# Kernel optimization log

Measured on AMD Instinct MI355X. Metric: run time of the kernel, lower is better.

The kernel has to match this reference:

```python
import jax, jax.numpy as jnp
import numpy as np

N_NODES = 100000
N_EDGES = 1600000
N_GRAPHS = 1000
NODES_PER_GRAPH = 100  # batch vector is arange(N)//100: exactly 100 nodes per graph
HID = 32
MAX_Z = 1000
K = 30
D_LAT = HID * 3 + 1  # 97, total_latent_dim


def setup_inputs() -> dict:
    key = jax.random.key(0)
    ks = jax.random.split(key, 24)
    s = 1.0 / np.sqrt(HID)
    inp = {
        "z": jax.random.randint(ks[0], (N_NODES,), 0, MAX_Z, dtype=jnp.int32),
        "edge_index": jax.random.randint(ks[1], (2, N_EDGES), 0, N_NODES, dtype=jnp.int32),
        "batch": (jnp.arange(N_NODES, dtype=jnp.int32) // NODES_PER_GRAPH),
        "edge_weight": jax.random.uniform(ks[2], (N_EDGES,), jnp.float32, 0.1, 1.0),
        "z_emb": jax.random.normal(ks[3], (MAX_Z, HID), jnp.float32) * 0.1,
        # GCNConv stack: [32->32, 32->32, 32->32, 32->1]
        "Wg1": jax.random.normal(ks[4], (HID, HID)) * s,
        "bg1": jnp.zeros((HID,), jnp.float32),
        "Wg2": jax.random.normal(ks[5], (HID, HID)) * s,
        "bg2": jnp.zeros((HID,), jnp.float32),
        "Wg3": jax.random.normal(ks[6], (HID, HID)) * s,
        "bg3": jnp.zeros((HID,), jnp.float32),
        "Wg4": jax.random.normal(ks[7], (HID, 1)) * s,
        "bg4": jnp.zeros((1,), jnp.float32),
        # Conv1d(1, 16, kernel=97, stride=97)
        "Wc1": jax.random.normal(ks[8], (16, D_LAT)) * (1.0 / np.sqrt(D_LAT)),
        "bc1": jnp.zeros((16,), jnp.float32),
        # Conv1d(16, 32, kernel=5, stride=1)
        "Wc2": jax.random.normal(ks[9], (32, 16, 5)) * (1.0 / np.sqrt(16 * 5)),
        "bc2": jnp.zeros((32,), jnp.float32),
        # Linear(352, 128), Linear(128, 1)
        "Wl1": jax.random.normal(ks[10], (352, 128)) * (1.0 / np.sqrt(352)),
        "bl1": jnp.zeros((128,), jnp.float32),
        "Wl2": jax.random.normal(ks[11], (128, 1)) * (1.0 / np.sqrt(128)),
        "bl2": jnp.zeros((1,), jnp.float32),
    }
    return inp


def gcn_conv(x, src, dst, ew, W, b, n):
    # PyG GCNConv: xW, add self-loops (weight 1), sym-normalize, aggregate at dst, + bias
    xw = x @ W
    deg = jax.ops.segment_sum(ew, dst, num_segments=n) + 1.0  # +1 for self loop
    dinv = jnp.where(deg > 0, jax.lax.rsqrt(deg), 0.0)
    norm = dinv[src] * ew * dinv[dst]                          # [E]
    out = jax.ops.segment_sum(norm[:, None] * xw[src], dst, num_segments=n)
    out = out + xw * (dinv * dinv)[:, None]                    # self-loop term
    return out + b


def _forward(z, edge_index, batch, edge_weight, z_emb, Wg1, bg1, Wg2, bg2, Wg3, bg3,
             Wg4, bg4, Wc1, bc1, Wc2, bc2, Wl1, bl1, Wl2, bl2):
    src, dst = edge_index[0], edge_index[1]
    n = z.shape[0]
    x = z_emb[z]                                              # [N, 32]
    xs = []
    h = x
    for W, b in ((Wg1, bg1), (Wg2, bg2), (Wg3, bg3), (Wg4, bg4)):
        h = jnp.tanh(gcn_conv(h, src, dst, edge_weight, W, b, n))
        xs.append(h)
    x = jnp.concatenate(xs, axis=-1)                          # [N, 97]
    # global_sort_pool: batch is uniform (100 nodes/graph) so dense batching is a reshape
    dense = x.reshape(N_GRAPHS, NODES_PER_GRAPH, D_LAT)       # [B, 100, 97]
    idx = jnp.argsort(-dense[:, :, -1], axis=1)[:, :K]        # sort desc by last channel
    top = jnp.take_along_axis(dense, idx[:, :, None], axis=1)  # [B, 30, 97]
    # Conv1d(1,16,97,stride=97) on flattened [B,1,30*97] == per-slot dense layer
    y = jax.nn.relu(jnp.einsum('bkd,cd->bck', top, Wc1) + bc1[None, :, None])  # [B,16,30]
    y = y.reshape(N_GRAPHS, 16, K // 2, 2).max(axis=-1)        # MaxPool1d(2,2) -> [B,16,15]
    y = jax.lax.conv_general_dilated(y, Wc2, (1,), 'VALID',
                                     dimension_numbers=('NCH', 'OIH', 'NCH'))
    y = jax.nn.relu(y + bc2[None, :, None])                    # [B,32,11]
    y = y.reshape(N_GRAPHS, -1)                                # [B,352]
    y = jax.nn.relu(y @ Wl1 + bl1)                             # dropout: eval mode, identity
    return y @ Wl2 + bl2                                       # [B,1]


def reference(z, edge_index, batch, edge_weight, z_emb, Wg1, bg1, Wg2, bg2, Wg3, bg3,
              Wg4, bg4, Wc1, bc1, Wc2, bc2, Wl1, bl1, Wl2, bl2):
    return _forward(z, edge_index, batch, edge_weight, z_emb, Wg1, bg1, Wg2, bg2, Wg3,
                    bg3, Wg4, bg4, Wc1, bc1, Wc2, bc2, Wl1, bl1, Wl2, bl2)
```

## Files before the change

kernel.cpp:

```cpp
#include <hip/hip_runtime.h>

#define HID 32
#define DLAT 97
#define NPG 100
#define TOPK 30
#define BKT_NODES 128
#define BKT_SHIFT 7
#define NBUCK 1024
#define CAPF 2432
#define CHUNK 8192

__global__ __launch_bounds__(256) void binB1_kernel(
    const int* __restrict__ src, const int* __restrict__ dst,
    const float* __restrict__ ew, int* __restrict__ gcursor,
    int2* __restrict__ bedge, int E) {
    __shared__ int hist[NBUCK];
    __shared__ int lcur[NBUCK];
    __shared__ int dcache[CHUNK];
    for (int i = threadIdx.x; i < NBUCK; i += 256) hist[i] = 0;
    __syncthreads();
    int base = blockIdx.x * CHUNK;
    int M = min(E - base, CHUNK);
    for (int i = threadIdx.x; i < M; i += 256) {
        int d = dst[base + i];
        dcache[i] = d;
        atomicAdd(&hist[d >> BKT_SHIFT], 1);
    }
    __syncthreads();
    for (int b = threadIdx.x; b < NBUCK; b += 256) {
        int v = hist[b];
        lcur[b] = b * CAPF + (v ? atomicAdd(&gcursor[b], v) : 0);
    }
    __syncthreads();
    for (int i = threadIdx.x; i < M; i += 256) {
        int d = dcache[i];
        int slot = atomicAdd(&lcur[d >> BKT_SHIFT], 1);
        bedge[slot] = make_int2(src[base + i] | ((d & (BKT_NODES - 1)) << 20),
                                __float_as_int(ew[base + i]));
    }
}

__global__ __launch_bounds__(256) void sortlocal2_kernel(
    const int2* __restrict__ bedge, const int* __restrict__ gcursor,
    const int* __restrict__ z, const float* __restrict__ z_emb,
    const float* __restrict__ W1, int2* __restrict__ csr,
    int* __restrict__ row_start, int* __restrict__ row_deg,
    float* __restrict__ dinv, float* __restrict__ xw_a, int N) {
    __shared__ int2 LDSe[CAPF];
    __shared__ int sh256[256];
    __shared__ int cnt[BKT_NODES];
    __shared__ int sh2[BKT_NODES];
    __shared__ int lc2[BKT_NODES];
    __shared__ int zloc[BKT_NODES];
    __shared__ float dloc[BKT_NODES];
    __shared__ float W1L[HID * HID];
    __shared__ int bstart_s;

    int b = blockIdx.x, t = threadIdx.x;

    int t4 = t * 4;
    int a0 = gcursor[t4], a1 = gcursor[t4 + 1], a2 = gcursor[t4 + 2], a3 = gcursor[t4 + 3];
    int tsum = a0 + a1 + a2 + a3;
    sh256[t] = tsum;
    for (int i = t; i < HID * HID; i += 256) W1L[i] = W1[i];
    if (t < BKT_NODES) cnt[t] = 0;
    __syncthreads();
    for (int off = 1; off < 256; off <<= 1) {
        int tv = (t >= off) ? sh256[t - off] : 0;
        __syncthreads();
        sh256[t] += tv;
        __syncthreads();
    }
    if (t == (b >> 2)) {
        int e = sh256[t] - tsum;
        int bb = b & 3;
        if (bb > 0) e += a0;
        if (bb > 1) e += a1;
        if (bb > 2) e += a2;
        bstart_s = e;
    }
    __syncthreads();
    const int begOut = bstart_s;
    const int M = gcursor[b];

    for (int i = t; i < M; i += 256) {
        int2 e = bedge[(size_t)b * CAPF + i];
        LDSe[i] = e;
        atomicAdd(&cnt[(e.x >> 20) & (BKT_NODES - 1)], 1);
    }
    __syncthreads();
    int v = 0, excl = 0;
    int n = b * BKT_NODES + t;
    if (t < BKT_NODES) { v = cnt[t]; sh2[t] = v; }
    __syncthreads();
    for (int off = 1; off < BKT_NODES; off <<= 1) {
        int tv = (t >= off && t < BKT_NODES) ? sh2[t - off] : 0;
        __syncthreads();
        if (t < BKT_NODES) sh2[t] += tv;
        __syncthreads();
    }
    if (t < BKT_NODES) {
        excl = sh2[t] - v;
        lc2[t] = excl;
        if (n < N) {
            row_start[n] = begOut + excl;
            row_deg[n] = v;
        }
    }
    __syncthreads();
    for (int i = t; i < M; i += 256) {
        int2 e = LDSe[i];
        int slot = atomicAdd(&lc2[(e.x >> 20) & (BKT_NODES - 1)], 1);
        csr[begOut + slot] = make_int2(e.x & 0xFFFFF, e.y);
    }
    __syncthreads();
    if (t < BKT_NODES && n < N) {
        float s = 1.f;
        int s0 = begOut + excl;
        for (int i = 0; i < v; ++i) s += __int_as_float(csr[s0 + i].y);
        float di = 1.f / sqrtf(s);
        dinv[n] = di;
        dloc[t] = di;
        zloc[t] = z[n];
    }
    __syncthreads();
    int lim = min(BKT_NODES, N - b * BKT_NODES);
    if (lim > 0) {
        for (int idx = t; idx < lim * HID; idx += 256) {
            int nl = idx >> 5, f = idx & 31;
            const float* row = z_emb + (size_t)zloc[nl] * HID;
            float s = 0.f;
#pragma unroll
            for (int k = 0; k < HID; ++k) s += row[k] * W1L[k * HID + f];
            xw_a[(size_t)(b * BKT_NODES + nl) * HID + f] = s * dloc[nl];
        }
    }
}

template <int MODE>
__global__ __launch_bounds__(256) void agg32f_kernel(
    const int* __restrict__ row_start, const int* __restrict__ row_deg,
    const int2* __restrict__ csr, const float* __restrict__ xw,
    const float* __restrict__ b, const float* __restrict__ dinv,
    const float* __restrict__ Wn, float* __restrict__ concat, int col_off,
    float* __restrict__ xw_next, int N) {
    int tid = blockIdx.x * blockDim.x + threadIdx.x;
    int n = tid >> 5;
    if (n >= N) return;
    int f = threadIdx.x & 31;
    int beg = row_start[n];
    int end = beg + row_deg[n];
    float s0 = 0.f, s1 = 0.f;
    for (int i = beg; i < end; i += 8) {
        float w[8];
        int idx[8];
#pragma unroll
        for (int j = 0; j < 8; ++j) {
            int ii = min(i + j, end - 1);
            int2 v = csr[ii];
            idx[j] = v.x;
            w[j] = (i + j < end) ? __int_as_float(v.y) : 0.f;
        }
        float x[8];
#pragma unroll
        for (int j = 0; j < 8; ++j) x[j] = xw[(size_t)idx[j] * HID + f];
#pragma unroll
        for (int j = 0; j < 8; ++j) {
            if (j & 1) s1 += w[j] * x[j];
            else       s0 += w[j] * x[j];
        }
    }
    float s = s0 + s1;
    float di = dinv[n];
    float outv = tanhf(di * (s + xw[(size_t)n * HID + f]) + b[f]);
    concat[(size_t)n * DLAT + col_off + f] = outv;

    if (MODE == 0) {
        float p = 0.f;
#pragma unroll
        for (int k = 0; k < HID; ++k) {
            float ok = __shfl(outv, k, 32);
            p += ok * Wn[k * HID + f];
        }
        xw_next[(size_t)n * HID + f] = p * di;
    } else {
        float p = outv * Wn[f];
        p += __shfl_xor(p, 16);
        p += __shfl_xor(p, 8);
        p += __shfl_xor(p, 4);
        p += __shfl_xor(p, 2);
        p += __shfl_xor(p, 1);
        if (f == 0) xw_next[n] = p * di;
    }
}

__global__ __launch_bounds__(256) void topk_head_kernel(
    const int* __restrict__ row_start, const int* __restrict__ row_deg,
    const int2* __restrict__ csr, const float* __restrict__ xw4,
    const float* __restrict__ b4, const float* __restrict__ dinv,
    const float* __restrict__ concat,
    const float* __restrict__ Wc1, const float* __restrict__ bc1,
    const float* __restrict__ Wc2, const float* __restrict__ bc2,
    const float* __restrict__ Wl1, const float* __restrict__ bl1,
    const float* __restrict__ Wl2, const float* __restrict__ bl2,
    float* __restrict__ out) {
    int g = blockIdx.x;
    int tid = threadIdx.x;
    __shared__ float v[NPG];
    __shared__ int tidx[TOPK];
    __shared__ float tval[TOPK];
    __shared__ float top[TOPK * DLAT];
    __shared__ float Wc1L[16 * DLAT];
    __shared__ float Wc2L[32 * 16 * 5];
    __shared__ float y1[16 * TOPK];
    __shared__ float y2[16 * 15];
    __shared__ float y3[352];
    __shared__ float r[256];

    for (int i = tid; i < 16 * DLAT; i += 256) Wc1L[i] = Wc1[i];
    for (int i = tid; i < 32 * 16 * 5; i += 256) Wc2L[i] = Wc2[i];

    if (tid < NPG) {
        int n = g * NPG + tid;
        int beg = row_start[n], end = beg + row_deg[n];
        float s0 = 0.f, s1 = 0.f;
        for (int i = beg; i < end; i += 4) {
            int2 e0 = csr[min(i, end - 1)];
            int2 e1 = csr[min(i + 1, end - 1)];
            int2 e2 = csr[min(i + 2, end - 1)];
            int2 e3 = csr[min(i + 3, end - 1)];
            float x0 = xw4[e0.x], x1 = xw4[e1.x], x2 = xw4[e2.x], x3 = xw4[e3.x];
            s0 += __int_as_float(e0.y) * x0;
            if (i + 1 < end) s1 += __int_as_float(e1.y) * x1;
            if (i + 2 < end) s0 += __int_as_float(e2.y) * x2;
            if (i + 3 < end) s1 += __int_as_float(e3.y) * x3;
        }
        v[tid] = tanhf(dinv[n] * ((s0 + s1) + xw4[n]) + b4[0]);
    }
    __syncthreads();
    if (tid < NPG) {
        float vi = v[tid];
        int cnt = 0;
#pragma unroll 4
        for (int j = 0; j < NPG; ++j) {
            float vj = v[j];
            cnt += (vj > vi) || (vj == vi && j < tid);
        }
        if (cnt < TOPK) {
            tidx[cnt] = g * NPG + tid;
            tval[cnt] = vi;
        }
    }
    __syncthreads();

    for (int idx = tid; idx < TOPK * DLAT; idx += 256) {
        int k = idx / DLAT, d = idx - k * DLAT;
        top[idx] = (d == 96) ? tval[k] : concat[(size_t)tidx[k] * DLAT + d];
    }
    __syncthreads();

    for (int idx = tid; idx < 16 * TOPK; idx += 256) {
        int c = idx / TOPK, k = idx % TOPK;
        float s = bc1[c];
        const float* w = Wc1L + c * DLAT;
        const float* t = top + k * DLAT;
#pragma unroll 4
        for (int d = 0; d < DLAT; ++d) s += t[d] * w[d];
        y1[c * TOPK + k] = fmaxf(s, 0.f);
    }
    __syncthreads();

    for (int idx = tid; idx < 16 * 15; idx += 256) {
        int c = idx / 15, j = idx % 15;
        y2[idx] = fmaxf(y1[c * TOPK + 2 * j], y1[c * TOPK + 2 * j + 1]);
    }
    __syncthreads();

    for (int idx = tid; idx < 352; idx += 256) {
        int o = idx / 11, t = idx % 11;
        float s = bc2[o];
#pragma unroll
        for (int i = 0; i < 16; ++i) {
#pragma unroll
            for (int k = 0; k < 5; ++k)
                s += Wc2L[(o * 16 + i) * 5 + k] * y2[i * 15 + t + k];
        }
        y3[idx] = fmaxf(s, 0.f);
    }
    __syncthreads();

    {
        int half = tid >> 7;
        int o = tid & 127;
        int d0 = half * 176;
        float s = (half == 0) ? bl1[o] : 0.f;
#pragma unroll 1
        for (int d = d0; d < d0 + 176; d += 8) {
            float wv[8], yv[8];
#pragma unroll
            for (int j = 0; j < 8; ++j) wv[j] = Wl1[(d + j) * 128 + o];
#pragma unroll
            for (int j = 0; j < 8; ++j) yv[j] = y3[d + j];
#pragma unroll
            for (int j = 0; j < 8; ++j) s += yv[j] * wv[j];
        }
        r[tid] = s;
    }
    __syncthreads();
    if (tid < 128) r[tid] = fmaxf(r[tid] + r[tid + 128], 0.f) * Wl2[tid];
    __syncthreads();
    if (tid < 64) r[tid] += r[tid + 64];
    __syncthreads();
    if (tid == 0) {
        float s = 0.f;
        for (int j = 0; j < 64; ++j) s += r[j];
        out[g] = s + bl2[0];
    }
}


extern "C" void kernel_launch(void* const* d_in, const int* in_sizes, int n_in,
                              void* d_out, int out_size, void* d_ws, size_t ws_size,
                              hipStream_t stream) {
    const int* z = (const int*)d_in[0];
    const int* ei = (const int*)d_in[1];
    const float* ew = (const float*)d_in[3];
    const float* z_emb = (const float*)d_in[4];
    const float* Wg[4] = {(const float*)d_in[5], (const float*)d_in[7],
                          (const float*)d_in[9], (const float*)d_in[11]};
    const float* bg[4] = {(const float*)d_in[6], (const float*)d_in[8],
                          (const float*)d_in[10], (const float*)d_in[12]};
    const float* Wc1 = (const float*)d_in[13];
    const float* bc1 = (const float*)d_in[14];
    const float* Wc2 = (const float*)d_in[15];
    const float* bc2 = (const float*)d_in[16];
    const float* Wl1 = (const float*)d_in[17];
    const float* bl1 = (const float*)d_in[18];
    const float* Wl2 = (const float*)d_in[19];
    const float* bl2 = (const float*)d_in[20];
    float* out = (float*)d_out;

    const int N = in_sizes[0];
    const int E = in_sizes[1] / 2;
    const int G = out_size;
    const int* src = ei;
    const int* dst = ei + E;

    auto cdiv = [](long long a, long long b) { return (int)((a + b - 1) / b); };
    const int NB = cdiv(E, CHUNK);
    const int NBKT = cdiv(N, BKT_NODES);

    char* ws = (char*)d_ws;
    int2* bedge = (int2*)ws;                  ws += sizeof(int2) * (size_t)NBUCK * CAPF;
    int2* csr = (int2*)ws;                    ws += sizeof(int2) * (size_t)E;
    int* gcursor = (int*)ws;                  ws += sizeof(int) * NBUCK;
    int* row_start = (int*)ws;                ws += sizeof(int) * N;
    int* row_deg = (int*)ws;                  ws += sizeof(int) * N;
    float* dinv = (float*)ws;                 ws += sizeof(float) * N;
    float* xw_a = (float*)ws;                 ws += sizeof(float) * (size_t)N * HID;
    float* concat = (float*)ws;               ws += sizeof(float) * (size_t)N * DLAT;
    float* xw4 = (float*)ws;                  ws += sizeof(float) * N;
    float* xw_b = (float*)bedge;

    const int B = 256;

    hipMemsetAsync(gcursor, 0, sizeof(int) * NBUCK, stream);
    binB1_kernel<<<NB, B, 0, stream>>>(src, dst, ew, gcursor, bedge, E);
    sortlocal2_kernel<<<NBKT, B, 0, stream>>>(bedge, gcursor, z, z_emb, Wg[0], csr,
                                              row_start, row_deg, dinv, xw_a, N);

    const int AGGB = cdiv((long long)N * 32, B);
    agg32f_kernel<0><<<AGGB, B, 0, stream>>>(row_start, row_deg, csr, xw_a, bg[0], dinv,
                                             Wg[1], concat, 0, xw_b, N);
    agg32f_kernel<0><<<AGGB, B, 0, stream>>>(row_start, row_deg, csr, xw_b, bg[1], dinv,
                                             Wg[2], concat, 32, xw_a, N);
    agg32f_kernel<1><<<AGGB, B, 0, stream>>>(row_start, row_deg, csr, xw_a, bg[2], dinv,
                                             Wg[3], concat, 64, xw4, N);

    topk_head_kernel<<<G, 256, 0, stream>>>(row_start, row_deg, csr, xw4, bg[3], dinv,
                                            concat, Wc1, bc1, Wc2, bc2, Wl1, bl1,
                                            Wl2, bl2, out);
}
```

Measured before the change: 380.6 us.

## Vectorize edge gathers with float4 lanes and split out dense xW GEMM

The aggregation kernel now has each group of 4 lanes process different edges and gather float4 slices of the neighbor row, followed by a shuffle reduction. This replaces per-lane scalar loads and should raise memory-level parallelism. The next-layer xW product moves out of the aggregation kernel into a separate per-node GEMM kernel that keeps W in shared memory, replacing the 32-step shuffle loop. The concat buffer changes from a strided 97-wide row to three contiguous 32-wide blocks, which gives coalesced stores at the cost of two extra launches and an extra round trip of the hidden state through memory.

```diff
diff --git a/kernel.cpp b/kernel.cpp
--- a/kernel.cpp
+++ b/kernel.cpp
@@ -138,59 +138,101 @@
 }
 
 template <int MODE>
-__global__ __launch_bounds__(256) void agg32f_kernel(
+__global__ __launch_bounds__(256) void agg32v_kernel(
     const int* __restrict__ row_start, const int* __restrict__ row_deg,
     const int2* __restrict__ csr, const float* __restrict__ xw,
     const float* __restrict__ b, const float* __restrict__ dinv,
-    const float* __restrict__ Wn, float* __restrict__ concat, int col_off,
-    float* __restrict__ xw_next, int N) {
+    const float* __restrict__ Wn, float* __restrict__ cout,
+    float* __restrict__ xw4, int N) {
     int tid = blockIdx.x * blockDim.x + threadIdx.x;
     int n = tid >> 5;
     if (n >= N) return;
-    int f = threadIdx.x & 31;
+    int lane = threadIdx.x & 31;
+    int eq = lane & 3;
+    int f4 = lane & 28;
     int beg = row_start[n];
     int end = beg + row_deg[n];
-    float s0 = 0.f, s1 = 0.f;
-    for (int i = beg; i < end; i += 8) {
-        float w[8];
-        int idx[8];
-#pragma unroll
-        for (int j = 0; j < 8; ++j) {
-            int ii = min(i + j, end - 1);
-            int2 v = csr[ii];
-            idx[j] = v.x;
-            w[j] = (i + j < end) ? __int_as_float(v.y) : 0.f;
-        }
-        float x[8];
-#pragma unroll
-        for (int j = 0; j < 8; ++j) x[j] = xw[(size_t)idx[j] * HID + f];
-#pragma unroll
-        for (int j = 0; j < 8; ++j) {
-            if (j & 1) s1 += w[j] * x[j];
-            else       s0 += w[j] * x[j];
-        }
-    }
-    float s = s0 + s1;
+    float4 acc = make_float4(0.f, 0.f, 0.f, 0.f);
+    for (int i = beg; i < end; i += 16) {
+        int2 cw[4];
+        float w[4];
+#pragma unroll
+        for (int j = 0; j < 4; ++j) {
+            int e = i + 4 * j + eq;
+            cw[j] = csr[min(e, end - 1)];
+            w[j] = (e < end) ? __int_as_float(cw[j].y) : 0.f;
+        }
+        float4 x[4];
+#pragma unroll
+        for (int j = 0; j < 4; ++j)
+            x[j] = *(const float4*)(xw + (size_t)cw[j].x * HID + f4);
+#pragma unroll
+        for (int j = 0; j < 4; ++j) {
+            acc.x += w[j] * x[j].x;
+            acc.y += w[j] * x[j].y;
+            acc.z += w[j] * x[j].z;
+            acc.w += w[j] * x[j].w;
+        }
+    }
+#pragma unroll
+    for (int m = 1; m <= 2; m <<= 1) {
+        acc.x += __shfl_xor(acc.x, m, 32);
+        acc.y += __shfl_xor(acc.y, m, 32);
+        acc.z += __shfl_xor(acc.z, m, 32);
+        acc.w += __shfl_xor(acc.w, m, 32);
+    }
+    float s = (eq == 0) ? acc.x : (eq == 1) ? acc.y : (eq == 2) ? acc.z : acc.w;
     float di = dinv[n];
-    float outv = tanhf(di * (s + xw[(size_t)n * HID + f]) + b[f]);
-    concat[(size_t)n * DLAT + col_off + f] = outv;
-
-    if (MODE == 0) {
-        float p = 0.f;
-#pragma unroll
-        for (int k = 0; k < HID; ++k) {
-            float ok = __shfl(outv, k, 32);
-            p += ok * Wn[k * HID + f];
-        }
-        xw_next[(size_t)n * HID + f] = p * di;
-    } else {
-        float p = outv * Wn[f];
-        p += __shfl_xor(p, 16);
-        p += __shfl_xor(p, 8);
-        p += __shfl_xor(p, 4);
-        p += __shfl_xor(p, 2);
-        p += __shfl_xor(p, 1);
-        if (f == 0) xw_next[n] = p * di;
+    float outv = tanhf(di * (s + xw[(size_t)n * HID + lane]) + b[lane]);
+    cout[(size_t)n * HID + lane] = outv;
+
+    if (MODE == 1) {
+        float p = outv * Wn[lane];
+        p += __shfl_xor(p, 16, 32);
+        p += __shfl_xor(p, 8, 32);
+        p += __shfl_xor(p, 4, 32);
+        p += __shfl_xor(p, 2, 32);
+        p += __shfl_xor(p, 1, 32);
+        if (lane == 0) xw4[n] = p * di;
+    }
+}
+
+__global__ __launch_bounds__(256) void xwgemm_kernel(
+    const float* __restrict__ h, const float* __restrict__ Wn,
+    const float* __restrict__ dinv, float* __restrict__ xw_next, int N) {
+    __shared__ float4 WnL[HID * 8];
+    int tid = threadIdx.x;
+    WnL[tid] = ((const float4*)Wn)[tid];
+    __syncthreads();
+    int n = blockIdx.x * 256 + tid;
+    if (n >= N) return;
+    const float4* hr = (const float4*)(h + (size_t)n * HID);
+    float4 acc[8];
+#pragma unroll
+    for (int fb = 0; fb < 8; ++fb) acc[fb] = make_float4(0.f, 0.f, 0.f, 0.f);
+#pragma unroll
+    for (int k4 = 0; k4 < 8; ++k4) {
+        float4 h4 = hr[k4];
+#pragma unroll
+        for (int kk = 0; kk < 4; ++kk) {
+            float hk = (kk == 0) ? h4.x : (kk == 1) ? h4.y : (kk == 2) ? h4.z : h4.w;
+            int k = k4 * 4 + kk;
+#pragma unroll
+            for (int fb = 0; fb < 8; ++fb) {
+                float4 w4 = WnL[k * 8 + fb];
+                acc[fb].x += hk * w4.x;
+                acc[fb].y += hk * w4.y;
+                acc[fb].z += hk * w4.z;
+                acc[fb].w += hk * w4.w;
+            }
+        }
+    }
+    float di = dinv[n];
+    float4* o = (float4*)(xw_next + (size_t)n * HID);
+#pragma unroll
+    for (int fb = 0; fb < 8; ++fb) {
+        acc[fb].x *= di; acc[fb].y *= di; acc[fb].z *= di; acc[fb].w *= di;
+        o[fb] = acc[fb];
     }
 }
 
@@ -198,12 +240,12 @@
     const int* __restrict__ row_start, const int* __restrict__ row_deg,
     const int2* __restrict__ csr, const float* __restrict__ xw4,
     const float* __restrict__ b4, const float* __restrict__ dinv,
-    const float* __restrict__ concat,
+    const float* __restrict__ cblk,
     const float* __restrict__ Wc1, const float* __restrict__ bc1,
     const float* __restrict__ Wc2, const float* __restrict__ bc2,
     const float* __restrict__ Wl1, const float* __restrict__ bl1,
     const float* __restrict__ Wl2, const float* __restrict__ bl2,
-    float* __restrict__ out) {
+    float* __restrict__ out, int N) {
     int g = blockIdx.x;
     int tid = threadIdx.x;
     __shared__ float v[NPG];
@@ -255,7 +297,10 @@
 
     for (int idx = tid; idx < TOPK * DLAT; idx += 256) {
         int k = idx / DLAT, d = idx - k * DLAT;
-        top[idx] = (d == 96) ? tval[k] : concat[(size_t)tidx[k] * DLAT + d];
+        float val;
+        if (d == 96) val = tval[k];
+        else val = cblk[(size_t)(d >> 5) * N * HID + (size_t)tidx[k] * HID + (d & 31)];
+        top[idx] = val;
     }
     __syncthreads();
 
@@ -358,9 +403,12 @@
     int* row_deg = (int*)ws;                  ws += sizeof(int) * N;
     float* dinv = (float*)ws;                 ws += sizeof(float) * N;
     float* xw_a = (float*)ws;                 ws += sizeof(float) * (size_t)N * HID;
-    float* concat = (float*)ws;               ws += sizeof(float) * (size_t)N * DLAT;
+    float* cblk = (float*)ws;                 ws += sizeof(float) * (size_t)3 * N * HID;
     float* xw4 = (float*)ws;                  ws += sizeof(float) * N;
     float* xw_b = (float*)bedge;
+    float* cb0 = cblk;
+    float* cb1 = cblk + (size_t)N * HID;
+    float* cb2 = cblk + (size_t)2 * N * HID;
 
     const int B = 256;
 
@@ -370,14 +418,17 @@
                                               row_start, row_deg, dinv, xw_a, N);
 
     const int AGGB = cdiv((long long)N * 32, B);
-    agg32f_kernel<0><<<AGGB, B, 0, stream>>>(row_start, row_deg, csr, xw_a, bg[0], dinv,
-                                             Wg[1], concat, 0, xw_b, N);
-    agg32f_kernel<0><<<AGGB, B, 0, stream>>>(row_start, row_deg, csr, xw_b, bg[1], dinv,
-                                             Wg[2], concat, 32, xw_a, N);
-    agg32f_kernel<1><<<AGGB, B, 0, stream>>>(row_start, row_deg, csr, xw_a, bg[2], dinv,
-                                             Wg[3], concat, 64, xw4, N);
+    const int GEMB = cdiv(N, B);
+    agg32v_kernel<0><<<AGGB, B, 0, stream>>>(row_start, row_deg, csr, xw_a, bg[0], dinv,
+                                             Wg[1], cb0, nullptr, N);
+    xwgemm_kernel<<<GEMB, B, 0, stream>>>(cb0, Wg[1], dinv, xw_b, N);
+    agg32v_kernel<0><<<AGGB, B, 0, stream>>>(row_start, row_deg, csr, xw_b, bg[1], dinv,
+                                             Wg[2], cb1, nullptr, N);
+    xwgemm_kernel<<<GEMB, B, 0, stream>>>(cb1, Wg[2], dinv, xw_a, N);
+    agg32v_kernel<1><<<AGGB, B, 0, stream>>>(row_start, row_deg, csr, xw_a, bg[2], dinv,
+                                             Wg[3], cb2, xw4, N);
 
     topk_head_kernel<<<G, 256, 0, stream>>>(row_start, row_deg, csr, xw4, bg[3], dinv,
-                                            concat, Wc1, bc1, Wc2, bc2, Wl1, bl1,
-                                            Wl2, bl2, out);
-}
+                                            cblk, Wc1, bc1, Wc2, bc2, Wl1, bl1,
+                                            Wl2, bl2, out, N);
+}
```

After: 382.1 us. Within noise of the previous version (+0.4%).
